# Performance work log

Measured on AMD Instinct MI355X. Metric: run time of the kernel, lower is better.

Reference implementation:

```python
import jax, jax.numpy as jnp
import numpy as np

N_USERS = 100000
M_ITEMS = 200000
N_NODES = N_USERS + M_ITEMS
N_EDGES = 1200000
D = 64
N_LAYERS = 3
BATCH = 4096


def setup_inputs() -> dict:
    key = jax.random.key(0)
    ks = jax.random.split(key, 11)
    return {
        "users": jax.random.randint(ks[0], (BATCH,), 0, N_USERS),
        "items": jax.random.randint(ks[1], (BATCH,), 0, M_ITEMS),
        "rows": jax.random.randint(ks[2], (N_EDGES,), 0, N_NODES),
        "cols": jax.random.randint(ks[3], (N_EDGES,), 0, N_NODES),
        "vals": jax.random.uniform(ks[4], (N_EDGES,), dtype=jnp.float32),
        "user_emb": jax.random.normal(ks[5], (N_USERS, D), dtype=jnp.float32) * 0.1,
        "item_emb": jax.random.normal(ks[6], (M_ITEMS, D), dtype=jnp.float32) * 0.1,
        "W_gc": jax.random.normal(ks[7], (N_LAYERS, D, D), dtype=jnp.float32) * 0.1,
        "b_gc": jax.random.normal(ks[8], (N_LAYERS, D), dtype=jnp.float32) * 0.1,
        "W_bi": jax.random.normal(ks[9], (N_LAYERS, D, D), dtype=jnp.float32) * 0.1,
        "b_bi": jax.random.normal(ks[10], (N_LAYERS, D), dtype=jnp.float32) * 0.1,
    }


def _spmm(rows, cols, vals, x):
    # sparse.mm(Graph, x): out[r] = sum_e vals[e] * x[cols[e]] for rows[e]==r
    gathered = vals[:, None] * x[cols]  # [E, D]
    return jax.ops.segment_sum(gathered, rows, num_segments=N_NODES)


def _computer(rows, cols, vals, user_emb, item_emb, W_gc, b_gc, W_bi, b_bi):
    ego = jnp.concatenate([user_emb, item_emb], axis=0)  # [N, D]
    embs = [ego]
    for k in range(N_LAYERS):
        side = _spmm(rows, cols, vals, ego)
        sum_emb = side @ W_gc[k] + b_gc[k]
        bi_emb = (ego * side) @ W_bi[k] + b_bi[k]
        ego = jax.nn.leaky_relu(sum_emb + bi_emb, negative_slope=0.2)
        nrm = jnp.linalg.norm(ego, axis=1, keepdims=True)
        ego = ego / jnp.maximum(nrm, 1e-12)
        embs.append(ego)
    mean_emb = jnp.mean(jnp.stack(embs, axis=1), axis=1)  # [N, D]
    return mean_emb[:N_USERS], mean_emb[N_USERS:]


def reference(users, items, rows, cols, vals, user_emb, item_emb, W_gc, b_gc, W_bi, b_bi):
    all_users, all_items = _computer(rows, cols, vals, user_emb, item_emb, W_gc, b_gc, W_bi, b_bi)
    u = all_users[users]  # [B, D]
    i = all_items[items]  # [B, D]
    return jnp.sum(u * i, axis=1)  # [B]
```

## Files before the change

kernel.cpp:

```cpp
#include <hip/hip_runtime.h>
#include <hip/hip_bf16.h>

#define N_USERS 100000
#define M_ITEMS 200000
#define N_NODES 300000
#define N_EDGES 1200000
#define BATCH   4096
#define NB      ((N_NODES + 255) / 256)
#define CHUNK   5
#define EPT4    (N_EDGES / 4)
#define EGRID4  ((EPT4 + 255) / 256)

typedef __attribute__((ext_vector_type(8))) short short8;
typedef __attribute__((ext_vector_type(4))) float floatx4;

static __device__ __forceinline__ float b2f(__hip_bfloat16 x) { return __bfloat162float(x); }

static __device__ __forceinline__ short f2bs(float f) {
    union { __hip_bfloat16 h; short s; } u;
    u.h = __float2bfloat16(f);
    return u.s;
}
static __device__ __forceinline__ float us2f(unsigned int us) {
    return __uint_as_float(us << 16);
}

static __device__ __forceinline__ float loadf(const void* p, int i, int isbf) {
    if (isbf) return b2f(((const __hip_bfloat16*)p)[i]);
    return ((const float*)p)[i];
}

static __device__ __forceinline__ int sniff_dev(const void* vals) {
    const unsigned short* v16 = (const unsigned short*)vals;
    int c = 0;
#pragma unroll
    for (int i = 0; i < 16; ++i) {
        unsigned int ub = (v16[2 * i] >> 8) & 0xFF;
        if (ub >= 0x3A && ub <= 0x3F) ++c;
    }
    return (c >= 12) ? 1 : 0;
}

static __device__ __forceinline__ void unpack8(float* o, uint4 e) {
    unsigned int w[4] = {e.x, e.y, e.z, e.w};
#pragma unroll
    for (int j = 0; j < 8; ++j) o[j] = us2f((w[j >> 1] >> ((j & 1) * 16)) & 0xFFFFu);
}

static __device__ __forceinline__ const unsigned short* bfsrc(
    const void* ue, const void* ie, int n64) {
    return (n64 < N_USERS * 64)
        ? (const unsigned short*)ue + (size_t)(unsigned)n64
        : (const unsigned short*)ie + (size_t)(unsigned)(n64 - N_USERS * 64);
}
static __device__ __forceinline__ const float* fsrc(
    const void* ue, const void* ie, int n64) {
    return (n64 < N_USERS * 64)
        ? (const float*)ue + (size_t)(unsigned)n64
        : (const float*)ie + (size_t)(unsigned)(n64 - N_USERS * 64);
}

static __device__ __forceinline__ void gather16o(
    float* o0, float* o1, const unsigned short* ego,
    const void* ue, const void* ie, int n64, int quad, int isbf, int use_src) {
    if (!use_src) {
        const unsigned short* p = ego + (size_t)(unsigned)n64 + quad * 8;
        unpack8(o0, *(const uint4*)p);
        unpack8(o1, *(const uint4*)(p + 32));
    } else if (isbf) {
        const unsigned short* p = bfsrc(ue, ie, n64) + quad * 8;
        unpack8(o0, *(const uint4*)p);
        unpack8(o1, *(const uint4*)(p + 32));
    } else {
        const float* p = fsrc(ue, ie, n64) + quad * 8;
        float4 a = *(const float4*)p;
        float4 b = *(const float4*)(p + 4);
        float4 c = *(const float4*)(p + 32);
        float4 d = *(const float4*)(p + 36);
        o0[0]=a.x; o0[1]=a.y; o0[2]=a.z; o0[3]=a.w; o0[4]=b.x; o0[5]=b.y; o0[6]=b.z; o0[7]=b.w;
        o1[0]=c.x; o1[1]=c.y; o1[2]=c.z; o1[3]=c.w; o1[4]=d.x; o1[5]=d.y; o1[6]=d.z; o1[7]=d.w;
    }
}

static __device__ __forceinline__ void fma8x2(
    float* s0, float* s1, float v, uint4 a, uint4 b) {
    float t0[8], t1[8];
    unpack8(t0, a);
    unpack8(t1, b);
#pragma unroll
    for (int j = 0; j < 8; ++j) {
        s0[j] = fmaf(v, t0[j], s0[j]);
        s1[j] = fmaf(v, t1[j], s1[j]);
    }
}

static __device__ __forceinline__ void fma8x2f(
    float* s0, float* s1, float v, float4 a, float4 b, float4 c, float4 d) {
    s0[0]=fmaf(v,a.x,s0[0]); s0[1]=fmaf(v,a.y,s0[1]); s0[2]=fmaf(v,a.z,s0[2]); s0[3]=fmaf(v,a.w,s0[3]);
    s0[4]=fmaf(v,b.x,s0[4]); s0[5]=fmaf(v,b.y,s0[5]); s0[6]=fmaf(v,b.z,s0[6]); s0[7]=fmaf(v,b.w,s0[7]);
    s1[0]=fmaf(v,c.x,s1[0]); s1[1]=fmaf(v,c.y,s1[1]); s1[2]=fmaf(v,c.z,s1[2]); s1[3]=fmaf(v,c.w,s1[3]);
    s1[4]=fmaf(v,d.x,s1[4]); s1[5]=fmaf(v,d.y,s1[5]); s1[6]=fmaf(v,d.z,s1[6]); s1[7]=fmaf(v,d.w,s1[7]);
}

__global__ __launch_bounds__(256) void setup_kernel(
    const void* __restrict__ Wg, const void* __restrict__ bg,
    const void* __restrict__ Wb, const void* __restrict__ bb,
    const void* __restrict__ vals,
    const int* __restrict__ users, const int* __restrict__ items,
    unsigned short* __restrict__ WT, float* __restrict__ sb,
    unsigned char* __restrict__ f1, unsigned char* __restrict__ f2,
    unsigned char* __restrict__ f3) {
    if (blockIdx.x < 12) {
        int isbf = __builtin_amdgcn_readfirstlane(sniff_dev(vals));
        int t = blockIdx.x * 256 + threadIdx.x;
        if (t < 3072) {
            int lane = t & 63, h = (t >> 6) & 1, ct = (t >> 7) & 3, w = (t >> 9) & 1, k = t >> 10;
            int m = lane & 15, quad = lane >> 4;
            const void* Wsrc = w ? Wb : Wg;
#pragma unroll
            for (int j = 0; j < 8; ++j) {
                int kk = h * 32 + quad * 8 + j;
                WT[(size_t)(k * 1024 + w * 512 + ct * 128 + h * 64 + lane) * 8 + j] =
                    (unsigned short)f2bs(loadf(Wsrc, k * 4096 + kk * 64 + ct * 16 + m, isbf));
            }
        }
        if (t < 192) sb[t] = loadf(bg, t, isbf) + loadf(bb, t, isbf);
    } else {
        int i = (blockIdx.x - 12) * 256 + threadIdx.x;
        int n = -1;
        if (i < BATCH) n = users[i];
        else if (i < 2 * BATCH) n = N_USERS + items[i - BATCH];
        if (n >= 0) { f1[n] = 1; f2[n] = 1; f3[n] = 1; }
    }
}

__global__ __launch_bounds__(256) void prop_kernel(
    const int4* __restrict__ rows4, const int4* __restrict__ cols4,
    const unsigned char* __restrict__ src, unsigned char* __restrict__ dst) {
    int t = blockIdx.x * 256 + threadIdx.x;
    if (t < EPT4) {
        int4 r = rows4[t];
        int4 c = cols4[t];
        if (src[r.x]) dst[c.x] = 1;
        if (src[r.y]) dst[c.y] = 1;
        if (src[r.z]) dst[c.z] = 1;
        if (src[r.w]) dst[c.w] = 1;
    }
}

__global__ __launch_bounds__(256) void count_rank_kernel(
    const int4* __restrict__ rows4, const unsigned char* __restrict__ flag1,
    int* __restrict__ off, uint2* __restrict__ rank) {
    int t = blockIdx.x * 256 + threadIdx.x;
    if (t < EPT4) {
        int4 r = rows4[t];
        unsigned int k0 = 0xFFFFu, k1 = 0xFFFFu, k2 = 0xFFFFu, k3 = 0xFFFFu;
        if (flag1[r.x]) k0 = (unsigned int)atomicAdd(&off[r.x + 1], 1);
        if (flag1[r.y]) k1 = (unsigned int)atomicAdd(&off[r.y + 1], 1);
        if (flag1[r.z]) k2 = (unsigned int)atomicAdd(&off[r.z + 1], 1);
        if (flag1[r.w]) k3 = (unsigned int)atomicAdd(&off[r.w + 1], 1);
        rank[t] = make_uint2((k0 & 0xFFFFu) | (k1 << 16), (k2 & 0xFFFFu) | (k3 << 16));
    }
}

static __device__ __forceinline__ int deg_class(int d) {
    return d >= 16 ? 0 : d >= 8 ? 1 : d >= 4 ? 2 : 3;
}

__global__ __launch_bounds__(256) void scanA_kernel(
    const int* __restrict__ off, const unsigned char* __restrict__ flags,
    int* __restrict__ bsum, int* __restrict__ bcnt, unsigned char* __restrict__ cls) {
    __shared__ int s[256];
    __shared__ int w[4];
    int t = threadIdx.x;
    int n = blockIdx.x * 256 + t;
    bool ir = (n < N_NODES);
    int deg = ir ? off[n + 1] : 0;
    s[t] = deg;
    __syncthreads();
    for (int o = 128; o >= 1; o >>= 1) {
        if (t < o) s[t] += s[t + o];
        __syncthreads();
    }
    if (t == 0) bsum[blockIdx.x] = s[0];
    int c = deg_class(deg);
    if (ir) cls[n] = (unsigned char)c;
    int lane = t & 63;
    int wid  = t >> 6;
#pragma unroll
    for (int L = 0; L < 3; ++L) {
        bool fl = ir && flags[L * N_NODES + n];
#pragma unroll
        for (int cc = 0; cc < 4; ++cc) {
            unsigned long long mask = __ballot(fl && (c == cc));
            if (lane == 0) w[wid] = __popcll(mask);
            __syncthreads();
            if (t == 0) bcnt[(L * 4 + cc) * NB + blockIdx.x] = w[0] + w[1] + w[2] + w[3];
            __syncthreads();
        }
    }
}

__global__ __launch_bounds__(256) void scanB_kernel(
    int* __restrict__ bsum, int* __restrict__ bcnt, int* __restrict__ cnts) {
    __shared__ int s[256];
    int t = threadIdx.x;
    {
        int base = t * CHUNK, loc = 0;
        for (int j = 0; j < CHUNK; ++j) { int i = base + j; if (i < NB) loc += bsum[i]; }
        s[t] = loc;
        __syncthreads();
        for (int o = 1; o < 256; o <<= 1) {
            int add = (t >= o) ? s[t - o] : 0;
            __syncthreads();
            s[t] += add;
            __syncthreads();
        }
        int run = (t == 0) ? 0 : s[t - 1];
        for (int j = 0; j < CHUNK; ++j) {
            int i = base + j;
            if (i < NB) { int tmp = bsum[i]; bsum[i] = run; run += tmp; }
        }
        __syncthreads();
    }
    for (int L = 0; L < 3; ++L) {
        int levelRun = 0;
        for (int c = 0; c < 4; ++c) {
            int v = L * 4 + c;
            int base = t * CHUNK;
            int loc = 0;
            for (int j = 0; j < CHUNK; ++j) { int i = base + j; if (i < NB) loc += bcnt[v * NB + i]; }
            s[t] = loc;
            __syncthreads();
            for (int o = 1; o < 256; o <<= 1) {
                int add = (t >= o) ? s[t - o] : 0;
                __syncthreads();
                s[t] += add;
                __syncthreads();
            }
            int run = ((t == 0) ? 0 : s[t - 1]) + levelRun;
            int total = s[255];
            for (int j = 0; j < CHUNK; ++j) {
                int i = base + j;
                if (i < NB) { int tmp = bcnt[v * NB + i]; bcnt[v * NB + i] = run; run += tmp; }
            }
            levelRun += total;
            __syncthreads();
        }
        if (t == 0) cnts[L] = levelRun;
    }
}

__global__ __launch_bounds__(256) void scanC_kernel(
    int* __restrict__ off, const int* __restrict__ bsum,
    const unsigned char* __restrict__ flags, const unsigned char* __restrict__ cls,
    const int* __restrict__ bcnt, int* __restrict__ lists, int* __restrict__ map3) {
    __shared__ int s[256];
    __shared__ int wsum[4];
    int t = threadIdx.x;
    int n = blockIdx.x * 256 + t;
    bool ir = (n < N_NODES);
    s[t] = ir ? off[n + 1] : 0;
    __syncthreads();
    for (int o = 1; o < 256; o <<= 1) {
        int add = (t >= o) ? s[t - o] : 0;
        __syncthreads();
        s[t] += add;
        __syncthreads();
    }
    if (ir) off[n + 1] = s[t] + bsum[blockIdx.x];
    int c = ir ? (int)cls[n] : 3;
    int lane = t & 63;
    int wid  = t >> 6;
#pragma unroll
    for (int L = 0; L < 3; ++L) {
        bool fl = ir && flags[L * N_NODES + n];
#pragma unroll
        for (int cc = 0; cc < 4; ++cc) {
            bool f = fl && (c == cc);
            unsigned long long mask = __ballot(f);
            if (lane == 0) wsum[wid] = __popcll(mask);
            __syncthreads();
            int base = bcnt[(L * 4 + cc) * NB + blockIdx.x];
            for (int i = 0; i < wid; ++i) base += wsum[i];
            if (f) {
                int pos = base + __popcll(mask & ((1ull << lane) - 1ull));
                lists[L * N_NODES + pos] = n;
                if (L == 2) map3[n] = pos + 1;
            }
            __syncthreads();
        }
    }
}

__global__ __launch_bounds__(256) void fill_kernel(
    const int4* __restrict__ rows4, const int4* __restrict__ cols4,
    const void* __restrict__ vals, const int* __restrict__ off,
    const uint2* __restrict__ rank, int2* __restrict__ epack) {
    int isbf = __builtin_amdgcn_readfirstlane(sniff_dev(vals));
    int t = blockIdx.x * 256 + threadIdx.x;
    if (t < EPT4) {
        int4 r = rows4[t];
        int4 c = cols4[t];
        uint2 kk = rank[t];
        unsigned int k0 = kk.x & 0xFFFFu, k1 = kk.x >> 16;
        unsigned int k2 = kk.y & 0xFFFFu, k3 = kk.y >> 16;
        int e = t * 4;
        if (k0 != 0xFFFFu)
            epack[off[r.x] + (int)k0] = make_int2(c.x << 6, __float_as_int(loadf(vals, e, isbf)));
        if (k1 != 0xFFFFu)
            epack[off[r.y] + (int)k1] = make_int2(c.y << 6, __float_as_int(loadf(vals, e + 1, isbf)));
        if (k2 != 0xFFFFu)
            epack[off[r.z] + (int)k2] = make_int2(c.z << 6, __float_as_int(loadf(vals, e + 2, isbf)));
        if (k3 != 0xFFFFu)
            epack[off[r.w] + (int)k3] = make_int2(c.w << 6, __float_as_int(loadf(vals, e + 3, isbf)));
    }
}

template<int USE_SRC>
__global__ __launch_bounds__(256) void fused_layer_kernel(
    const int* __restrict__ off, const int2* __restrict__ epack,
    const unsigned short* __restrict__ ego_in,
    const void* __restrict__ ue, const void* __restrict__ ie,
    const void* __restrict__ vals,
    const unsigned short* __restrict__ WT, const float* __restrict__ sb,
    int klayer, unsigned short* __restrict__ ego_out,
    const int* __restrict__ list, const int* __restrict__ cntp,
    const int* __restrict__ map3, float* __restrict__ acc) {
    const int isbf = USE_SRC ? __builtin_amdgcn_readfirstlane(sniff_dev(vals)) : 0;
    const int cnt  = __builtin_amdgcn_readfirstlane(cntp[0]);
    const int ntile = (cnt + 15) >> 4;
    const int lane = threadIdx.x & 63;
    const int m    = lane & 15;
    const int quad = lane >> 4;

    const unsigned short* wt = WT + (size_t)klayer * 8192;
    short8 Bg[4][2], Bb[4][2];
#pragma unroll
    for (int ct = 0; ct < 4; ++ct)
#pragma unroll
        for (int h = 0; h < 2; ++h) {
            Bg[ct][h] = *(const short8*)(wt + (size_t)((ct * 2 + h) * 64 + lane) * 8);
            Bb[ct][h] = *(const short8*)(wt + (size_t)(512 + (ct * 2 + h) * 64 + lane) * 8);
        }
    float bv[4];
#pragma unroll
    for (int ct = 0; ct < 4; ++ct) bv[ct] = sb[klayer * 64 + ct * 16 + m];

    const int wv = blockIdx.x * 4 + (threadIdx.x >> 6);
    const int nw = gridDim.x * 4;
    for (int tile = wv; tile < ntile; tile += nw) {
        const int idx = tile * 16 + m;
        const int row = list[idx < cnt ? idx : cnt - 1];
        const int start = off[row];
        const int end   = off[row + 1];

        float eg0[8], eg1[8];
        gather16o(eg0, eg1, ego_in, ue, ie, row << 6, quad, isbf, USE_SRC);

        float s0[8] = {0,0,0,0,0,0,0,0};
        float s1[8] = {0,0,0,0,0,0,0,0};
        int e = start;
        if (!USE_SRC) {
            const unsigned short* eb = ego_in + quad * 8;
            for (; e + 4 <= end; e += 4) {
                int2 c0 = epack[e], c1 = epack[e + 1], c2 = epack[e + 2], c3 = epack[e + 3];
                const unsigned short* q0 = eb + (size_t)(unsigned)c0.x;
                const unsigned short* q1 = eb + (size_t)(unsigned)c1.x;
                const unsigned short* q2 = eb + (size_t)(unsigned)c2.x;
                const unsigned short* q3 = eb + (size_t)(unsigned)c3.x;
                uint4 a0 = *(const uint4*)q0, b0 = *(const uint4*)(q0 + 32);
                uint4 a1 = *(const uint4*)q1, b1 = *(const uint4*)(q1 + 32);
                uint4 a2 = *(const uint4*)q2, b2 = *(const uint4*)(q2 + 32);
                uint4 a3 = *(const uint4*)q3, b3 = *(const uint4*)(q3 + 32);
                fma8x2(s0, s1, __int_as_float(c0.y), a0, b0);
                fma8x2(s0, s1, __int_as_float(c1.y), a1, b1);
                fma8x2(s0, s1, __int_as_float(c2.y), a2, b2);
                fma8x2(s0, s1, __int_as_float(c3.y), a3, b3);
            }
        } else if (isbf) {
            for (; e + 4 <= end; e += 4) {
                int2 c0 = epack[e], c1 = epack[e + 1], c2 = epack[e + 2], c3 = epack[e + 3];
                const unsigned short* q0 = bfsrc(ue, ie, c0.x) + quad * 8;
                const unsigned short* q1 = bfsrc(ue, ie, c1.x) + quad * 8;
                const unsigned short* q2 = bfsrc(ue, ie, c2.x) + quad * 8;
                const unsigned short* q3 = bfsrc(ue, ie, c3.x) + quad * 8;
                uint4 a0 = *(const uint4*)q0, b0 = *(const uint4*)(q0 + 32);
                uint4 a1 = *(const uint4*)q1, b1 = *(const uint4*)(q1 + 32);
                uint4 a2 = *(const uint4*)q2, b2 = *(const uint4*)(q2 + 32);
                uint4 a3 = *(const uint4*)q3, b3 = *(const uint4*)(q3 + 32);
                fma8x2(s0, s1, __int_as_float(c0.y), a0, b0);
                fma8x2(s0, s1, __int_as_float(c1.y), a1, b1);
                fma8x2(s0, s1, __int_as_float(c2.y), a2, b2);
                fma8x2(s0, s1, __int_as_float(c3.y), a3, b3);
            }
        } else {
            for (; e + 2 <= end; e += 2) {
                int2 c0 = epack[e], c1 = epack[e + 1];
                const float* p0 = fsrc(ue, ie, c0.x) + quad * 8;
                const float* p1 = fsrc(ue, ie, c1.x) + quad * 8;
                float4 x0 = *(const float4*)p0, y0 = *(const float4*)(p0 + 4);
                float4 z0 = *(const float4*)(p0 + 32), w0 = *(const float4*)(p0 + 36);
                float4 x1 = *(const float4*)p1, y1 = *(const float4*)(p1 + 4);
                float4 z1 = *(const float4*)(p1 + 32), w1 = *(const float4*)(p1 + 36);
                fma8x2f(s0, s1, __int_as_float(c0.y), x0, y0, z0, w0);
                fma8x2f(s0, s1, __int_as_float(c1.y), x1, y1, z1, w1);
            }
        }
        for (; e < end; ++e) {
            int2 cv = epack[e];
            float v = __int_as_float(cv.y);
            float t0[8], t1[8];
            gather16o(t0, t1, ego_in, ue, ie, cv.x, quad, isbf, USE_SRC);
#pragma unroll
            for (int j = 0; j < 8; ++j) {
                s0[j] = fmaf(v, t0[j], s0[j]);
                s1[j] = fmaf(v, t1[j], s1[j]);
            }
        }

        short8 As0, As1, Ap0, Ap1;
#pragma unroll
        for (int j = 0; j < 8; ++j) {
            As0[j] = f2bs(s0[j]);
            As1[j] = f2bs(s1[j]);
            Ap0[j] = f2bs(eg0[j] * s0[j]);
            Ap1[j] = f2bs(eg1[j] * s1[j]);
        }

        floatx4 accf[4];
#pragma unroll
        for (int ct = 0; ct < 4; ++ct) {
            floatx4 a = {0.f, 0.f, 0.f, 0.f};
            a = __builtin_amdgcn_mfma_f32_16x16x32_bf16(As0, Bg[ct][0], a, 0, 0, 0);
            a = __builtin_amdgcn_mfma_f32_16x16x32_bf16(As1, Bg[ct][1], a, 0, 0, 0);
            a = __builtin_amdgcn_mfma_f32_16x16x32_bf16(Ap0, Bb[ct][0], a, 0, 0, 0);
            a = __builtin_amdgcn_mfma_f32_16x16x32_bf16(Ap1, Bb[ct][1], a, 0, 0, 0);
            accf[ct] = a;
        }

        float v[4][4];
        float ssq[4] = {0.f, 0.f, 0.f, 0.f};
#pragma unroll
        for (int ct = 0; ct < 4; ++ct)
#pragma unroll
            for (int r = 0; r < 4; ++r) {
                float x = accf[ct][r] + bv[ct];
                x = x > 0.f ? x : 0.2f * x;
                v[ct][r] = x;
                ssq[r] += x * x;
            }
#pragma unroll
        for (int o = 1; o < 16; o <<= 1)
#pragma unroll
            for (int r = 0; r < 4; ++r) ssq[r] += __shfl_xor(ssq[r], o, 64);
#pragma unroll
        for (int r = 0; r < 4; ++r) {
            int idx_w = tile * 16 + quad * 4 + r;
            if (idx_w < cnt) {
                float sc = 1.0f / fmaxf(sqrtf(ssq[r]), 1e-12f);
                int rw = list[idx_w];
                int c3 = map3[rw];
#pragma unroll
                for (int ct = 0; ct < 4; ++ct)
                    ego_out[(size_t)rw * 64 + ct * 16 + m] = (unsigned short)f2bs(v[ct][r] * sc);
                if (c3 > 0) {
                    float* ap = acc + (size_t)(c3 - 1) * 64 + m;
#pragma unroll
                    for (int ct = 0; ct < 4; ++ct) ap[ct * 16] += v[ct][r] * sc;
                }
            }
        }
    }
}

__global__ __launch_bounds__(256) void dot_kernel(
    const int* __restrict__ users, const int* __restrict__ items,
    const float* __restrict__ acc, const int* __restrict__ map3,
    const void* __restrict__ ue, const void* __restrict__ ie,
    void* __restrict__ out, const void* __restrict__ vals) {
    int isbf = __builtin_amdgcn_readfirstlane(sniff_dev(vals));
    int gid = blockIdx.x * 256 + threadIdx.x;
    int b = gid >> 6;
    int lane = gid & 63;
    int un = __builtin_amdgcn_readfirstlane(users[b]);
    int in_ = __builtin_amdgcn_readfirstlane(items[b]);
    int cu = __builtin_amdgcn_readfirstlane(map3[un]);
    int ci = __builtin_amdgcn_readfirstlane(map3[N_USERS + in_]);
    float u = (cu > 0 ? acc[(size_t)(cu - 1) * 64 + lane] : 0.f) + loadf(ue, un * 64 + lane, isbf);
    float v = (ci > 0 ? acc[(size_t)(ci - 1) * 64 + lane] : 0.f) + loadf(ie, in_ * 64 + lane, isbf);
    float pr = u * v;
#pragma unroll
    for (int o = 32; o >= 1; o >>= 1) pr += __shfl_xor(pr, o, 64);
    if (lane == 0) {
        float r = pr * 0.0625f;
        if (isbf) ((__hip_bfloat16*)out)[b] = __float2bfloat16(r);
        else      ((float*)out)[b] = r;
    }
}

static inline size_t align16(size_t x) { return (x + 15) & ~(size_t)15; }

extern "C" void kernel_launch(void* const* d_in, const int* in_sizes, int n_in,
                              void* d_out, int out_size, void* d_ws, size_t ws_size,
                              hipStream_t stream) {
    const int* users = (const int*)d_in[0];
    const int* items = (const int*)d_in[1];
    const int* rows  = (const int*)d_in[2];
    const int* cols  = (const int*)d_in[3];
    const void* vals     = d_in[4];
    const void* user_emb = d_in[5];
    const void* item_emb = d_in[6];
    const void* W_gc     = d_in[7];
    const void* b_gc     = d_in[8];
    const void* W_bi     = d_in[9];
    const void* b_bi     = d_in[10];

    const size_t egoB   = (size_t)N_NODES * 64 * sizeof(short);
    const size_t packB  = (size_t)N_EDGES * sizeof(int2);
    const size_t rankB  = (size_t)EPT4 * sizeof(uint2);
    const size_t bsumB  = (size_t)NB * sizeof(int);
    const size_t bcntB  = (size_t)12 * NB * sizeof(int);
    const size_t clsB   = (size_t)N_NODES;
    const size_t wtB    = (size_t)3 * 1024 * 8 * sizeof(short);
    const size_t sbB    = (size_t)192 * sizeof(float);
    const size_t accB   = (size_t)2 * BATCH * 64 * sizeof(float);
    const size_t offB   = (size_t)(N_NODES + 1) * sizeof(int);
    const size_t cntsB  = (size_t)4 * sizeof(int);
    const size_t map3B  = (size_t)N_NODES * sizeof(int);
    const size_t flagsB = (size_t)3 * N_NODES;

    char* ws = (char*)d_ws;
    size_t o = 0;
    unsigned short* egoA  = (unsigned short*)(ws + o); o += egoB;
    unsigned short* egoB2 = (unsigned short*)(ws + o); o += egoB;
    int2*  epack  = (int2*)(ws + o);  o += packB;
    uint2* rank   = (uint2*)(ws + o); o += rankB;
    int*   bsum   = (int*)(ws + o);   o += bsumB;
    int*   bcnt   = (int*)(ws + o);   o += bcntB;
    unsigned char* cls = (unsigned char*)(ws + o); o += clsB;
    o = align16(o);
    unsigned short* WT = (unsigned short*)(ws + o); o += wtB;
    float* sb     = (float*)(ws + o); o += sbB;
    o = align16(o);
    float* acc    = (float*)(ws + o);
    int*   off    = (int*)((char*)acc + accB);
    int*   cnts   = (int*)((char*)off + offB);
    int*   map3   = (int*)((char*)cnts + cntsB);
    unsigned char* flags = (unsigned char*)((char*)map3 + map3B);
    const size_t zeroB = accB + offB + cntsB + map3B + flagsB;
    unsigned char* flagL[3] = {flags, flags + N_NODES, flags + 2 * N_NODES};
    int* lists = (int*)(flags + flagsB);
    int* listL[3] = {lists, lists + N_NODES, lists + 2 * N_NODES};

    hipMemsetAsync(acc, 0, zeroB, stream);

    setup_kernel<<<44, 256, 0, stream>>>(W_gc, b_gc, W_bi, b_bi, vals, users, items,
                                         WT, sb, flagL[0], flagL[1], flagL[2]);

    prop_kernel<<<EGRID4, 256, 0, stream>>>((const int4*)rows, (const int4*)cols, flagL[2], flagL[1]);
    prop_kernel<<<EGRID4, 256, 0, stream>>>((const int4*)rows, (const int4*)cols, flagL[1], flagL[0]);

    count_rank_kernel<<<EGRID4, 256, 0, stream>>>((const int4*)rows, flagL[0], off, rank);

    scanA_kernel<<<NB, 256, 0, stream>>>(off, flags, bsum, bcnt, cls);
    scanB_kernel<<<1, 256, 0, stream>>>(bsum, bcnt, cnts);
    scanC_kernel<<<NB, 256, 0, stream>>>(off, bsum, flags, cls, bcnt, lists, map3);

    fill_kernel<<<EGRID4, 256, 0, stream>>>((const int4*)rows, (const int4*)cols, vals, off, rank, epack);

    fused_layer_kernel<1><<<2048, 256, 0, stream>>>(off, epack, egoA, user_emb, item_emb,
                                                    vals, WT, sb, 0, egoA,
                                                    listL[0], cnts + 0, map3, acc);
    fused_layer_kernel<0><<<2048, 256, 0, stream>>>(off, epack, egoA, user_emb, item_emb,
                                                    vals, WT, sb, 1, egoB2,
                                                    listL[1], cnts + 1, map3, acc);
    fused_layer_kernel<0><<<2048, 256, 0, stream>>>(off, epack, egoB2, user_emb, item_emb,
                                                    vals, WT, sb, 2, egoA,
                                                    listL[2], cnts + 2, map3, acc);
    dot_kernel<<<(BATCH * 64) / 256, 256, 0, stream>>>(users, items, acc, map3,
                                                       user_emb, item_emb, d_out, vals);
}
```

Measured before the change: 300.8 us.

## Use atomic tile tickets and reload weights per tile to cut register pressure

Replaces the static grid-stride tile loop in the fused layer kernel with dynamic work distribution through an atomic ticket counter, which balances the uneven per-row edge counts across waves. The MFMA weight fragments are no longer held in registers for the whole kernel; they are reloaded from global/L1 per tile. The self-embedding gather moves after the edge loop, and launch bounds request 6 blocks per CU with a smaller grid. Together these lower VGPR usage to raise occupancy for the latency-bound gather, at the cost of extra weight loads and one atomic per tile.

```diff
diff --git a/kernel.cpp b/kernel.cpp
--- a/kernel.cpp
+++ b/kernel.cpp
@@ -318,7 +318,7 @@
 }
 
 template<int USE_SRC>
-__global__ __launch_bounds__(256) void fused_layer_kernel(
+__global__ __launch_bounds__(256, 6) void fused_layer_kernel(
     const int* __restrict__ off, const int2* __restrict__ epack,
     const unsigned short* __restrict__ ego_in,
     const void* __restrict__ ue, const void* __restrict__ ie,
@@ -326,7 +326,8 @@
     const unsigned short* __restrict__ WT, const float* __restrict__ sb,
     int klayer, unsigned short* __restrict__ ego_out,
     const int* __restrict__ list, const int* __restrict__ cntp,
-    const int* __restrict__ map3, float* __restrict__ acc) {
+    const int* __restrict__ map3, float* __restrict__ acc,
+    int* __restrict__ ticket) {
     const int isbf = USE_SRC ? __builtin_amdgcn_readfirstlane(sniff_dev(vals)) : 0;
     const int cnt  = __builtin_amdgcn_readfirstlane(cntp[0]);
     const int ntile = (cnt + 15) >> 4;
@@ -335,28 +336,20 @@
     const int quad = lane >> 4;
 
     const unsigned short* wt = WT + (size_t)klayer * 8192;
-    short8 Bg[4][2], Bb[4][2];
-#pragma unroll
-    for (int ct = 0; ct < 4; ++ct)
-#pragma unroll
-        for (int h = 0; h < 2; ++h) {
-            Bg[ct][h] = *(const short8*)(wt + (size_t)((ct * 2 + h) * 64 + lane) * 8);
-            Bb[ct][h] = *(const short8*)(wt + (size_t)(512 + (ct * 2 + h) * 64 + lane) * 8);
-        }
     float bv[4];
 #pragma unroll
     for (int ct = 0; ct < 4; ++ct) bv[ct] = sb[klayer * 64 + ct * 16 + m];
 
-    const int wv = blockIdx.x * 4 + (threadIdx.x >> 6);
-    const int nw = gridDim.x * 4;
-    for (int tile = wv; tile < ntile; tile += nw) {
+    for (;;) {
+        int tile = 0;
+        if (lane == 0) tile = atomicAdd(ticket, 1);
+        tile = __shfl(tile, 0, 64);
+        if (tile >= ntile) break;
+
         const int idx = tile * 16 + m;
         const int row = list[idx < cnt ? idx : cnt - 1];
         const int start = off[row];
         const int end   = off[row + 1];
-
-        float eg0[8], eg1[8];
-        gather16o(eg0, eg1, ego_in, ue, ie, row << 6, quad, isbf, USE_SRC);
 
         float s0[8] = {0,0,0,0,0,0,0,0};
         float s1[8] = {0,0,0,0,0,0,0,0};
@@ -419,6 +412,9 @@
             }
         }
 
+        float eg0[8], eg1[8];
+        gather16o(eg0, eg1, ego_in, ue, ie, row << 6, quad, isbf, USE_SRC);
+
         short8 As0, As1, Ap0, Ap1;
 #pragma unroll
         for (int j = 0; j < 8; ++j) {
@@ -428,28 +424,27 @@
             Ap1[j] = f2bs(eg1[j] * s1[j]);
         }
 
-        floatx4 accf[4];
-#pragma unroll
-        for (int ct = 0; ct < 4; ++ct) {
-            floatx4 a = {0.f, 0.f, 0.f, 0.f};
-            a = __builtin_amdgcn_mfma_f32_16x16x32_bf16(As0, Bg[ct][0], a, 0, 0, 0);
-            a = __builtin_amdgcn_mfma_f32_16x16x32_bf16(As1, Bg[ct][1], a, 0, 0, 0);
-            a = __builtin_amdgcn_mfma_f32_16x16x32_bf16(Ap0, Bb[ct][0], a, 0, 0, 0);
-            a = __builtin_amdgcn_mfma_f32_16x16x32_bf16(Ap1, Bb[ct][1], a, 0, 0, 0);
-            accf[ct] = a;
-        }
-
         float v[4][4];
         float ssq[4] = {0.f, 0.f, 0.f, 0.f};
 #pragma unroll
-        for (int ct = 0; ct < 4; ++ct)
+        for (int ct = 0; ct < 4; ++ct) {
+            short8 Bg0 = *(const short8*)(wt + (size_t)((ct * 2 + 0) * 64 + lane) * 8);
+            short8 Bg1 = *(const short8*)(wt + (size_t)((ct * 2 + 1) * 64 + lane) * 8);
+            short8 Bb0 = *(const short8*)(wt + (size_t)(512 + (ct * 2 + 0) * 64 + lane) * 8);
+            short8 Bb1 = *(const short8*)(wt + (size_t)(512 + (ct * 2 + 1) * 64 + lane) * 8);
+            floatx4 a = {0.f, 0.f, 0.f, 0.f};
+            a = __builtin_amdgcn_mfma_f32_16x16x32_bf16(As0, Bg0, a, 0, 0, 0);
+            a = __builtin_amdgcn_mfma_f32_16x16x32_bf16(As1, Bg1, a, 0, 0, 0);
+            a = __builtin_amdgcn_mfma_f32_16x16x32_bf16(Ap0, Bb0, a, 0, 0, 0);
+            a = __builtin_amdgcn_mfma_f32_16x16x32_bf16(Ap1, Bb1, a, 0, 0, 0);
 #pragma unroll
             for (int r = 0; r < 4; ++r) {
-                float x = accf[ct][r] + bv[ct];
+                float x = a[r] + bv[ct];
                 x = x > 0.f ? x : 0.2f * x;
                 v[ct][r] = x;
                 ssq[r] += x * x;
             }
+        }
 #pragma unroll
         for (int o = 1; o < 16; o <<= 1)
 #pragma unroll
@@ -526,7 +521,7 @@
     const size_t sbB    = (size_t)192 * sizeof(float);
     const size_t accB   = (size_t)2 * BATCH * 64 * sizeof(float);
     const size_t offB   = (size_t)(N_NODES + 1) * sizeof(int);
-    const size_t cntsB  = (size_t)4 * sizeof(int);
+    const size_t cntsB  = (size_t)8 * sizeof(int);
     const size_t map3B  = (size_t)N_NODES * sizeof(int);
     const size_t flagsB = (size_t)3 * N_NODES;
 
@@ -546,6 +541,7 @@
     float* acc    = (float*)(ws + o);
     int*   off    = (int*)((char*)acc + accB);
     int*   cnts   = (int*)((char*)off + offB);
+    int*   tickets = cnts + 4;
     int*   map3   = (int*)((char*)cnts + cntsB);
     unsigned char* flags = (unsigned char*)((char*)map3 + map3B);
     const size_t zeroB = accB + offB + cntsB + map3B + flagsB;
@@ -569,15 +565,15 @@
 
     fill_kernel<<<EGRID4, 256, 0, stream>>>((const int4*)rows, (const int4*)cols, vals, off, rank, epack);
 
-    fused_layer_kernel<1><<<2048, 256, 0, stream>>>(off, epack, egoA, user_emb, item_emb,
+    fused_layer_kernel<1><<<1536, 256, 0, stream>>>(off, epack, egoA, user_emb, item_emb,
                                                     vals, WT, sb, 0, egoA,
-                                                    listL[0], cnts + 0, map3, acc);
-    fused_layer_kernel<0><<<2048, 256, 0, stream>>>(off, epack, egoA, user_emb, item_emb,
+                                                    listL[0], cnts + 0, map3, acc, tickets + 0);
+    fused_layer_kernel<0><<<1536, 256, 0, stream>>>(off, epack, egoA, user_emb, item_emb,
                                                     vals, WT, sb, 1, egoB2,
-                                                    listL[1], cnts + 1, map3, acc);
-    fused_layer_kernel<0><<<2048, 256, 0, stream>>>(off, epack, egoB2, user_emb, item_emb,
+                                                    listL[1], cnts + 1, map3, acc, tickets + 1);
+    fused_layer_kernel<0><<<1536, 256, 0, stream>>>(off, epack, egoB2, user_emb, item_emb,
                                                     vals, WT, sb, 2, egoA,
-                                                    listL[2], cnts + 2, map3, acc);
+                                                    listL[2], cnts + 2, map3, acc, tickets + 2);
     dot_kernel<<<(BATCH * 64) / 256, 256, 0, stream>>>(users, items, acc, map3,
                                                        user_emb, item_emb, d_out, vals);
 }
```

Result: slower. 580.5 us (+93.0%).
